# Optimization experiments

Hardware: AMD Instinct MI355X
Metric: run time of the kernel (lower is better)

## Reference

```python
import jax, jax.numpy as jnp
import numpy as np

N, E = 20000, 160000
NODE_DIM, EDGE_DIM, H, STEPS = 64, 16, 32, 3


def setup_inputs() -> dict:
    key = jax.random.key(0)
    ks = jax.random.split(key, 10)
    node_feat = jax.random.normal(ks[0], (N, NODE_DIM), dtype=jnp.float32)
    edge_index = jax.random.randint(ks[1], (2, E), 0, N, dtype=jnp.int32)
    edge_feat = jax.random.normal(ks[2], (E, EDGE_DIM), dtype=jnp.float32)
    # node_proj: Linear(node_dim, hidden)
    W_np = jax.random.normal(ks[3], (H, NODE_DIM), dtype=jnp.float32) / np.sqrt(NODE_DIM)
    b_np = jnp.zeros((H,), dtype=jnp.float32)
    # edge_net: Linear(edge_dim, hidden*hidden) -> reshape [E, H, H]
    W_e = jax.random.normal(ks[4], (H * H, EDGE_DIM), dtype=jnp.float32) / np.sqrt(EDGE_DIM)
    b_e = jnp.zeros((H * H,), dtype=jnp.float32)
    # GRUCell params (torch layout: [3H, H], gate order r, z, n)
    W_ih = jax.random.normal(ks[5], (3 * H, H), dtype=jnp.float32) / np.sqrt(H)
    W_hh = jax.random.normal(ks[6], (3 * H, H), dtype=jnp.float32) / np.sqrt(H)
    b_ih = jnp.zeros((3 * H,), dtype=jnp.float32)
    b_hh = jnp.zeros((3 * H,), dtype=jnp.float32)
    return {
        "node_feat": node_feat, "edge_index": edge_index, "edge_feat": edge_feat,
        "W_np": W_np, "b_np": b_np, "W_e": W_e, "b_e": b_e,
        "W_ih": W_ih, "W_hh": W_hh, "b_ih": b_ih, "b_hh": b_hh,
    }


def _gru_cell(x, h, W_ih, W_hh, b_ih, b_hh):
    gi = x @ W_ih.T + b_ih  # [N, 3H]
    gh = h @ W_hh.T + b_hh
    ir, iz, inn = jnp.split(gi, 3, axis=-1)
    hr, hz, hn = jnp.split(gh, 3, axis=-1)
    r = jax.nn.sigmoid(ir + hr)
    z = jax.nn.sigmoid(iz + hz)
    n = jnp.tanh(inn + r * hn)
    return (1.0 - z) * n + z * h


def reference(node_feat, edge_index, edge_feat, W_np, b_np, W_e, b_e, W_ih, W_hh, b_ih, b_hh):
    h = node_feat @ W_np.T + b_np                      # [N, H]
    A = (edge_feat @ W_e.T + b_e).reshape(-1, H, H)    # [E, H, H] per-edge matrices
    src, dst = edge_index[0], edge_index[1]
    for _ in range(STEPS):
        # m[v] += A[e] @ h[src[e]]  -> batched matvec + scatter-add
        msg = jnp.einsum('ehk,ek->eh', A, h[src])      # [E, H]
        m = jax.ops.segment_sum(msg, dst, num_segments=N)
        h = _gru_cell(m, h, W_ih, W_hh, b_ih, b_hh)
    return h
```

## Files before the change

kernel.cpp:

```cpp
#include <hip/hip_runtime.h>
#include <math.h>

#define N_NODES 20000
#define N_EDGES 160000
#define NODE_DIM 64
#define EDGE_DIM 16
#define H 32
#define STEPS 3

__global__ void hist_src_kernel(const int* __restrict__ ei, int* __restrict__ deg) {
    int e = blockIdx.x * 256 + threadIdx.x;
    if (e < N_EDGES) atomicAdd(&deg[ei[e]], 1);
}

__global__ void scan_a_kernel(const int* __restrict__ deg,
                              int* __restrict__ part, int* __restrict__ bsum) {
    __shared__ int s[256];
    int v = blockIdx.x * 256 + threadIdx.x;
    int x = (v < N_NODES) ? deg[v] : 0;
    s[threadIdx.x] = x;
    __syncthreads();
    for (int off = 1; off < 256; off <<= 1) {
        int t = (threadIdx.x >= off) ? s[threadIdx.x - off] : 0;
        __syncthreads();
        s[threadIdx.x] += t;
        __syncthreads();
    }
    if (v < N_NODES) part[v] = s[threadIdx.x] - x;
    if (threadIdx.x == 255) bsum[blockIdx.x] = s[255];
}

__global__ void scan_b_kernel(int* __restrict__ rowptr,
                              const int* __restrict__ bsum,
                              int* __restrict__ cursor) {
    __shared__ int boff[80];
    if (threadIdx.x == 0) {
        int run = 0;
        for (int b = 0; b < 79; ++b) { boff[b] = run; run += bsum[b]; }
    }
    __syncthreads();
    for (int v = threadIdx.x; v < N_NODES; v += 256) {
        int r = rowptr[v] + boff[v >> 8];
        rowptr[v] = r;
        cursor[v] = r;
    }
    if (threadIdx.x == 0) rowptr[N_NODES] = N_EDGES;
}

__global__ void fill_src_kernel(const int* __restrict__ ei,
                                const float* __restrict__ ef,
                                int* __restrict__ cursor,
                                int2* __restrict__ sd2,
                                float* __restrict__ ef2) {
    int e = blockIdx.x * 256 + threadIdx.x;
    if (e < N_EDGES) {
        int s = ei[e];
        int slot = atomicAdd(&cursor[s], 1);
        sd2[slot] = make_int2(s, ei[N_EDGES + e]);
        const float4* __restrict__ srcp = (const float4*)(ef + (size_t)e * EDGE_DIM);
        float4* __restrict__ dstp       = (float4*)(ef2 + (size_t)slot * EDGE_DIM);
        float4 a = srcp[0], b = srcp[1], c = srcp[2], d = srcp[3];
        dstp[0] = a; dstp[1] = b; dstp[2] = c; dstp[3] = d;
    }
}

__global__ void node_proj_kernel(const float* __restrict__ nf,
                                 const float* __restrict__ W,
                                 const float* __restrict__ b,
                                 float* __restrict__ h) {
    int tid = blockIdx.x * blockDim.x + threadIdx.x;
    if (tid >= N_NODES * H) return;
    int v = tid >> 5;
    int i = tid & 31;
    const float* __restrict__ row = nf + v * NODE_DIM;
    const float* __restrict__ w   = W + i * NODE_DIM;
    float acc = b[i];
#pragma unroll
    for (int d = 0; d < NODE_DIM; ++d) acc = fmaf(row[d], w[d], acc);
    h[tid] = acc;
}

__global__ __launch_bounds__(576)
void fused_msg_kernel(const float* __restrict__ We,
                      const float* __restrict__ be,
                      const float* __restrict__ h,
                      const int* __restrict__ rowptr,
                      const int2* __restrict__ sd2,
                      const float* __restrict__ ef2,
                      float* __restrict__ m) {
    __shared__ float hs[16 * 32];
    __shared__ float Ul[16 * 576];

    int t = threadIdx.x;

    float wreg[32];
    int p = -1;
    if (t < 512) {
        int L = t >> 4, q = (t >> 2) & 3, e = t & 3;
        int d = t & 15;
#pragma unroll
        for (int k = 0; k < H; ++k) wreg[k] = We[(L * H + k) * EDGE_DIM + d];
        p = q * 136 + L * 4 + e;
    } else if (t < 544) {
        int i = t - 512;
#pragma unroll
        for (int k = 0; k < H; ++k) wreg[k] = be[i * H + k];
        p = 544 + i;
    }

    int v0 = blockIdx.x * 16;

    if (t < 512) hs[t] = h[(size_t)v0 * H + t];
    __syncthreads();

    if (p >= 0) {
        for (int n = 0; n < 16; n += 2) {
            const float4* __restrict__ hp0 = (const float4*)(hs + n * H);
            const float4* __restrict__ hp1 = (const float4*)(hs + (n + 1) * H);
            float a0 = 0.f, a1 = 0.f;
#pragma unroll
            for (int kk = 0; kk < 8; ++kk) {
                float4 q0 = hp0[kk];
                float4 q1 = hp1[kk];
                a0 = fmaf(wreg[4 * kk + 0], q0.x, a0);
                a1 = fmaf(wreg[4 * kk + 0], q1.x, a1);
                a0 = fmaf(wreg[4 * kk + 1], q0.y, a0);
                a1 = fmaf(wreg[4 * kk + 1], q1.y, a1);
                a0 = fmaf(wreg[4 * kk + 2], q0.z, a0);
                a1 = fmaf(wreg[4 * kk + 2], q1.z, a1);
                a0 = fmaf(wreg[4 * kk + 3], q0.w, a0);
                a1 = fmaf(wreg[4 * kk + 3], q1.w, a1);
            }
            Ul[n * 576 + p]       = a0;
            Ul[(n + 1) * 576 + p] = a1;
        }
    }
    __syncthreads();

    int hw    = t >> 5;
    int lane  = t & 31;
    int jbeg  = rowptr[v0];
    int jend  = rowptr[v0 + 16];
    int nE    = jend - jbeg;
    int chunk = (nE + 17) / 18;
    int ja    = jbeg + hw * chunk;
    int jz    = ja + chunk; if (jz > jend) jz = jend;

    if (ja < jz) {
        int s_prev = -1;
        float4 u0 = {0,0,0,0}, u1 = {0,0,0,0}, u2 = {0,0,0,0}, u3 = {0,0,0,0};
        float  bv = 0.f;

        int2 sd = sd2[ja];
        const float4* __restrict__ ep0 = (const float4*)(ef2 + (size_t)ja * EDGE_DIM);
        float4 e0 = ep0[0], e1 = ep0[1], e2 = ep0[2], e3 = ep0[3];

        for (int j = ja; j < jz; ++j) {
            int jn = (j + 1 < jz) ? (j + 1) : j;
            int2 sdn = sd2[jn];
            const float4* __restrict__ epn =
                (const float4*)(ef2 + (size_t)jn * EDGE_DIM);
            float4 f0 = epn[0], f1 = epn[1], f2 = epn[2], f3 = epn[3];

            if (sd.x != s_prev) {
                s_prev = sd.x;
                int ls = sd.x - v0;
                const float4* __restrict__ up = (const float4*)(Ul + ls * 576);
                u0 = up[0 * 34 + lane];
                u1 = up[1 * 34 + lane];
                u2 = up[2 * 34 + lane];
                u3 = up[3 * 34 + lane];
                bv = Ul[ls * 576 + 544 + lane];
            }

            float msg = bv;
            msg = fmaf(e0.x, u0.x, msg);
            msg = fmaf(e0.y, u0.y, msg);
            msg = fmaf(e0.z, u0.z, msg);
            msg = fmaf(e0.w, u0.w, msg);
            msg = fmaf(e1.x, u1.x, msg);
            msg = fmaf(e1.y, u1.y, msg);
            msg = fmaf(e1.z, u1.z, msg);
            msg = fmaf(e1.w, u1.w, msg);
            msg = fmaf(e2.x, u2.x, msg);
            msg = fmaf(e2.y, u2.y, msg);
            msg = fmaf(e2.z, u2.z, msg);
            msg = fmaf(e2.w, u2.w, msg);
            msg = fmaf(e3.x, u3.x, msg);
            msg = fmaf(e3.y, u3.y, msg);
            msg = fmaf(e3.z, u3.z, msg);
            msg = fmaf(e3.w, u3.w, msg);

            atomicAdd(&m[(size_t)sd.y * H + lane], msg);

            sd = sdn;
            e0 = f0; e1 = f1; e2 = f2; e3 = f3;
        }
    }
}

__global__ __launch_bounds__(256, 4)
void gru_kernel(const float* __restrict__ Wih,
                const float* __restrict__ Whh,
                const float* __restrict__ bih,
                const float* __restrict__ bhh,
                float* __restrict__ m,
                const float* __restrict__ h,
                float* __restrict__ hout) {
    __shared__ float xs[16 * 64];
    __shared__ float gs[16 * 32 * 5];

    int c = threadIdx.x & 127;
    float4 wc[16];
    if (c < 96) {
        const float4* p = (const float4*)(Wih + c * H);
#pragma unroll
        for (int q = 0; q < 8; ++q) wc[q] = p[q];
    } else {
#pragma unroll
        for (int q = 0; q < 8; ++q) wc[q] = make_float4(0.f, 0.f, 0.f, 0.f);
    }
    int hrow = (c < 64) ? c : ((c >= 96) ? (c - 32) : -1);
    if (hrow >= 0) {
        const float4* p = (const float4*)(Whh + hrow * H);
#pragma unroll
        for (int q = 0; q < 8; ++q) wc[8 + q] = p[q];
    } else {
#pragma unroll
        for (int q = 0; q < 8; ++q) wc[8 + q] = make_float4(0.f, 0.f, 0.f, 0.f);
    }
    float bias;
    if (c < 64)      bias = bih[c] + bhh[c];
    else if (c < 96) bias = bih[c];
    else             bias = bhh[c - 32];

    int g    = threadIdx.x >> 5;
    int lane = threadIdx.x & 31;
    int half = threadIdx.x >> 7;
    int ci   = c & 31;
    int gt   = c >> 5;

    int v0 = blockIdx.x * 16;
    {
#pragma unroll
        for (int nn = 0; nn < 2; ++nn) {
            int n = g + nn * 8;
            int v = v0 + n;
            float mv = m[(size_t)v * H + lane];
            m[(size_t)v * H + lane] = 0.f;
            xs[n * 64 + lane]      = mv;
            xs[n * 64 + 32 + lane] = h[(size_t)v * H + lane];
        }
        __syncthreads();

#pragma unroll
        for (int n = 0; n < 8; n += 2) {
            const float4* x0 = (const float4*)(xs + (half * 8 + n) * 64);
            const float4* x1 = (const float4*)(xs + (half * 8 + n + 1) * 64);
            float acc0 = bias, acc1 = bias;
#pragma unroll
            for (int q = 0; q < 16; ++q) {
                float4 w = wc[q];
                float4 a = x0[q];
                float4 b = x1[q];
                acc0 = fmaf(w.x, a.x, acc0); acc1 = fmaf(w.x, b.x, acc1);
                acc0 = fmaf(w.y, a.y, acc0); acc1 = fmaf(w.y, b.y, acc1);
                acc0 = fmaf(w.z, a.z, acc0); acc1 = fmaf(w.z, b.z, acc1);
                acc0 = fmaf(w.w, a.w, acc0); acc1 = fmaf(w.w, b.w, acc1);
            }
            gs[((half * 8 + n)     * 32 + ci) * 5 + gt] = acc0;
            gs[((half * 8 + n + 1) * 32 + ci) * 5 + gt] = acc1;
        }
        __syncthreads();

        for (int t = threadIdx.x; t < 16 * 32; t += 256) {
            int nl = t >> 5, ii = t & 31;
            const float* gp = gs + (size_t)t * 5;
            float rs = gp[0], zs = gp[1], in_ = gp[2], hn = gp[3];
            float hv = xs[nl * 64 + 32 + ii];
            float r   = 1.f / (1.f + __expf(-rs));
            float z   = 1.f / (1.f + __expf(-zs));
            float nn2 = tanhf(in_ + r * hn);
            hout[(size_t)(v0 + nl) * H + ii] = (1.f - z) * nn2 + z * hv;
        }
    }
}

extern "C" void kernel_launch(void* const* d_in, const int* in_sizes, int n_in,
                              void* d_out, int out_size, void* d_ws, size_t ws_size,
                              hipStream_t stream) {
    const float* node_feat = (const float*)d_in[0];
    const int*   edge_idx  = (const int*)  d_in[1];
    const float* edge_feat = (const float*)d_in[2];
    const float* W_np      = (const float*)d_in[3];
    const float* b_np      = (const float*)d_in[4];
    const float* W_e       = (const float*)d_in[5];
    const float* b_e       = (const float*)d_in[6];
    const float* W_ih      = (const float*)d_in[7];
    const float* W_hh      = (const float*)d_in[8];
    const float* b_ih      = (const float*)d_in[9];
    const float* b_hh      = (const float*)d_in[10];

    float* h      = (float*)d_ws;
    float* m      = h + (size_t)N_NODES * H;
    float* ef2    = m + (size_t)N_NODES * H;
    int* rowptr   = (int*)(ef2 + (size_t)N_EDGES * EDGE_DIM);
    int* cursor   = rowptr + (N_NODES + 1);
    int* bsum     = cursor + N_NODES;
    int2* sd2     = (int2*)(bsum + 81);
    float* out    = (float*)d_out;

    hipMemsetAsync(m, 0, (size_t)N_NODES * H * sizeof(float), stream);
    hipMemsetAsync(cursor, 0, N_NODES * sizeof(int), stream);
    hist_src_kernel<<<(N_EDGES + 255) / 256, 256, 0, stream>>>(edge_idx, cursor);
    scan_a_kernel<<<(N_NODES + 255) / 256, 256, 0, stream>>>(cursor, rowptr, bsum);
    scan_b_kernel<<<1, 256, 0, stream>>>(rowptr, bsum, cursor);
    fill_src_kernel<<<(N_EDGES + 255) / 256, 256, 0, stream>>>(edge_idx, edge_feat,
                                                               cursor, sd2, ef2);
    node_proj_kernel<<<(N_NODES * H + 255) / 256, 256, 0, stream>>>(
        node_feat, W_np, b_np, h);

    for (int step = 0; step < STEPS; ++step) {
        fused_msg_kernel<<<N_NODES / 16, 576, 0, stream>>>(
            W_e, b_e, h, rowptr, sd2, ef2, m);
        float* dst_h = (step == STEPS - 1) ? out : h;
        gru_kernel<<<N_NODES / 16, 256, 0, stream>>>(W_ih, W_hh, b_ih, b_hh,
                                                     m, h, dst_h);
    }
}
```

Baseline: 298.5 us.

## Split message accumulator into two buffers and process two node tiles per GRU block

The message kernel now scatters alternating edges into two separate accumulation buffers, selected by edge index parity, to spread atomic contention on the same destination addresses. The GRU kernel sums both buffers, zeroes them, and each block now handles two 16-node tiles, so it launches half as many blocks and reuses the weights it loaded into registers. The workspace layout is reordered so one memset clears both accumulators and the degree counters together. The cost is an extra read and write of the second buffer per step and an added barrier between tiles.

```diff
diff --git a/kernel.cpp b/kernel.cpp
--- a/kernel.cpp
+++ b/kernel.cpp
@@ -7,6 +7,7 @@
 #define EDGE_DIM 16
 #define H 32
 #define STEPS 3
+#define NH (N_NODES * H)
 
 __global__ void hist_src_kernel(const int* __restrict__ ei, int* __restrict__ deg) {
     int e = blockIdx.x * 256 + threadIdx.x;
@@ -191,7 +192,7 @@
             msg = fmaf(e3.z, u3.z, msg);
             msg = fmaf(e3.w, u3.w, msg);
 
-            atomicAdd(&m[(size_t)sd.y * H + lane], msg);
+            atomicAdd(&m[(size_t)(j & 1) * NH + (size_t)sd.y * H + lane], msg);
 
             sd = sdn;
             e0 = f0; e1 = f1; e2 = f2; e3 = f3;
@@ -240,16 +241,19 @@
     int ci   = c & 31;
     int gt   = c >> 5;
 
-    int v0 = blockIdx.x * 16;
-    {
+    for (int tile = 0; tile < 2; ++tile) {
+        int v0 = (blockIdx.x * 2 + tile) * 16;
+
 #pragma unroll
         for (int nn = 0; nn < 2; ++nn) {
             int n = g + nn * 8;
             int v = v0 + n;
-            float mv = m[(size_t)v * H + lane];
-            m[(size_t)v * H + lane] = 0.f;
+            size_t idx = (size_t)v * H + lane;
+            float mv = m[idx] + m[NH + idx];
+            m[idx]      = 0.f;
+            m[NH + idx] = 0.f;
             xs[n * 64 + lane]      = mv;
-            xs[n * 64 + 32 + lane] = h[(size_t)v * H + lane];
+            xs[n * 64 + 32 + lane] = h[idx];
         }
         __syncthreads();
 
@@ -283,6 +287,7 @@
             float nn2 = tanhf(in_ + r * hn);
             hout[(size_t)(v0 + nl) * H + ii] = (1.f - z) * nn2 + z * hv;
         }
+        __syncthreads();
     }
 }
 
@@ -302,16 +307,15 @@
     const float* b_hh      = (const float*)d_in[10];
 
     float* h      = (float*)d_ws;
-    float* m      = h + (size_t)N_NODES * H;
-    float* ef2    = m + (size_t)N_NODES * H;
-    int* rowptr   = (int*)(ef2 + (size_t)N_EDGES * EDGE_DIM);
-    int* cursor   = rowptr + (N_NODES + 1);
-    int* bsum     = cursor + N_NODES;
-    int2* sd2     = (int2*)(bsum + 81);
+    float* m      = h + (size_t)NH;
+    int* cursor   = (int*)(m + 2 * (size_t)NH);
+    int* rowptr   = cursor + N_NODES;
+    int* bsum     = rowptr + (N_NODES + 2);
+    int2* sd2     = (int2*)(bsum + 82);
+    float* ef2    = (float*)(sd2 + N_EDGES);
     float* out    = (float*)d_out;
 
-    hipMemsetAsync(m, 0, (size_t)N_NODES * H * sizeof(float), stream);
-    hipMemsetAsync(cursor, 0, N_NODES * sizeof(int), stream);
+    hipMemsetAsync(m, 0, (2 * (size_t)NH + N_NODES) * sizeof(float), stream);
     hist_src_kernel<<<(N_EDGES + 255) / 256, 256, 0, stream>>>(edge_idx, cursor);
     scan_a_kernel<<<(N_NODES + 255) / 256, 256, 0, stream>>>(cursor, rowptr, bsum);
     scan_b_kernel<<<1, 256, 0, stream>>>(rowptr, bsum, cursor);
@@ -324,7 +328,7 @@
         fused_msg_kernel<<<N_NODES / 16, 576, 0, stream>>>(
             W_e, b_e, h, rowptr, sd2, ef2, m);
         float* dst_h = (step == STEPS - 1) ? out : h;
-        gru_kernel<<<N_NODES / 16, 256, 0, stream>>>(W_ih, W_hh, b_ih, b_hh,
-                                                     m, h, dst_h);
-    }
-}
+        gru_kernel<<<625, 256, 0, stream>>>(W_ih, W_hh, b_ih, b_hh,
+                                            m, h, dst_h);
+    }
+}
```

Measured after the change: 292.2 us (median of 2 runs). -2.1%, faster.
